# Kernel tuning notes

Hardware: AMD Instinct MI355X
Metric: run time of the kernel (lower is better)

Reference implementation:

```python
import jax, jax.numpy as jnp
import numpy as np

NUM_GROUPS = 256


def _linear(x, w, b):
    return x @ w + b


def _layernorm(x, g, b, eps=1e-5):
    mu = jnp.mean(x, axis=-1, keepdims=True)
    var = jnp.mean((x - mu) ** 2, axis=-1, keepdims=True)
    return (x - mu) / jnp.sqrt(var + eps) * g + b


def setup_inputs() -> dict:
    key = jax.random.key(0)
    ks = jax.random.split(key, 12)
    B, N, C = 16, 8192, 3
    s = 0.02
    return {
        "xyz": jax.random.normal(ks[0], (B, N, C), jnp.float32),
        "labels": jax.random.randint(ks[1], (B, N), 0, NUM_GROUPS),
        # conv1: Linear(3,128) -> LayerNorm(128) -> ReLU -> Linear(128,256)
        "w1a": jax.random.normal(ks[2], (3, 128), jnp.float32) * s,
        "b1a": jnp.zeros((128,), jnp.float32),
        "g1": jnp.ones((128,), jnp.float32),
        "beta1": jnp.zeros((128,), jnp.float32),
        "w1b": jax.random.normal(ks[3], (128, 256), jnp.float32) * s,
        "b1b": jnp.zeros((256,), jnp.float32),
        # conv2: Linear(512,512) -> LayerNorm(512) -> ReLU -> Linear(512,256)
        "w2a": jax.random.normal(ks[4], (512, 512), jnp.float32) * s,
        "b2a": jnp.zeros((512,), jnp.float32),
        "g2": jnp.ones((512,), jnp.float32),
        "beta2": jnp.zeros((512,), jnp.float32),
        "w2b": jax.random.normal(ks[5], (512, 256), jnp.float32) * s,
        "b2b": jnp.zeros((256,), jnp.float32),
    }


def reference(xyz, labels, w1a, b1a, g1, beta1, w1b, b1b,
              w2a, b2a, g2, beta2, w2b, b2b):
    # per-batch segment reductions over cluster labels
    seg_sum = jax.vmap(lambda f, l: jax.ops.segment_sum(f, l, num_segments=NUM_GROUPS))
    seg_max = jax.vmap(lambda f, l: jax.ops.segment_max(f, l, num_segments=NUM_GROUPS))
    gather = jax.vmap(lambda p, l: p[l])  # [G,D],[N] -> [N,D]

    # centroids = per-cluster mean of xyz (converged kmeans centroids)
    counts = seg_sum(jnp.ones_like(xyz[..., :1]), labels)          # [B,G,1]
    centroids = seg_sum(xyz, labels) / jnp.maximum(counts, 1.0)    # [B,G,3]

    p_i = gather(centroids, labels)                                # [B,N,3]
    relative_xyz = xyz - p_i                                       # feature_type='dp'

    h = _linear(relative_xyz, w1a, b1a)
    h = jax.nn.relu(_layernorm(h, g1, beta1))
    h = _linear(h, w1b, b1b)                                       # [B,N,256]

    pooled = seg_max(h, labels)                                    # [B,G,256]
    pooled = jnp.where(jnp.isfinite(pooled), pooled, 0.0)          # empty groups -> 0
    repeated = gather(pooled, labels)                              # [B,N,256]

    cat = jnp.concatenate([repeated, h], axis=-1)                  # [B,N,512]
    h2 = _linear(cat, w2a, b2a)
    h2 = jax.nn.relu(_layernorm(h2, g2, beta2))
    h2 = _linear(h2, w2b, b2b)                                     # [B,N,256]

    out = seg_max(h2, labels)                                      # [B,G,256]
    out = jnp.where(jnp.isfinite(out), out, 0.0)
    return (centroids, out, p_i, labels)
```

## Files before the change

kernel.cpp:

```cpp
#include <hip/hip_runtime.h>
#include <hip/hip_bf16.h>

#define NB_  16
#define NPTS 8192
#define NG   256
#define NP   (NB_*NPTS)
#define NBLK (NP/64)

#define OFF_CENT 0
#define OFF_OUT  12288
#define OFF_PI   1060864
#define OFF_LAB  1454080

typedef unsigned short u16;
typedef __attribute__((ext_vector_type(8))) short bf16x8;
typedef __attribute__((ext_vector_type(4))) float f32x4;

static constexpr size_t WS_SUMS  = 0;
static constexpr size_t WS_A1    = 65536;
static constexpr size_t WS_H     = WS_A1   + (size_t)NP*128*2;
static constexpr size_t WS_PBF   = WS_H    + (size_t)NP*256*2;
static constexpr size_t WS_WT1   = WS_PBF  + (size_t)NB_*NG*256*2;
static constexpr size_t WS_WT2A  = WS_WT1  + (size_t)256*128*2;
static constexpr size_t WS_WT2B  = WS_WT2A + (size_t)512*512*2;
static constexpr size_t WS_PREP  = WS_WT2B + (size_t)256*512*2;
static constexpr size_t WS_OFFS  = WS_PREP + (size_t)NB_*NG*512*4;
static constexpr size_t WS_CNT   = WS_OFFS + (size_t)NB_*NG*4;
static constexpr size_t WS_CUR   = WS_CNT  + (size_t)NB_*NG*4;
static constexpr size_t WS_SPOS  = WS_CUR  + (size_t)NB_*NG*4;
static constexpr size_t WS_GLAB  = WS_SPOS + (size_t)NP*4;
static constexpr size_t WS_PF    = WS_GLAB + (size_t)NP*4;
static constexpr size_t WS_PL    = WS_PF   + (size_t)NBLK*256*4;
static constexpr size_t WS_DST   = WS_PL   + (size_t)NBLK*256*4;
static constexpr size_t WS_NEED  = WS_DST  + (size_t)NB_*NG*256*4;

__device__ __forceinline__ u16 f2bf_bits(float f){
  __hip_bfloat16 h = __float2bfloat16(f);
  union { __hip_bfloat16 h; u16 s; } u; u.h = h; return u.s;
}
__device__ __forceinline__ float bf_bits2f(u16 s){
  return __uint_as_float(((unsigned)s) << 16);
}

__device__ __forceinline__ void gload16(const void* g, void* l){
  __builtin_amdgcn_global_load_lds((const __attribute__((address_space(1))) void*)g,
                                   (__attribute__((address_space(3))) void*)l, 16, 0, 0);
}

__global__ void k_init(float* __restrict__ sums, int* __restrict__ cursor){
  int i = blockIdx.x*blockDim.x + threadIdx.x;
  if (i < NB_*NG*4) sums[i] = 0.f;
  if (i < NB_*NG) cursor[i] = 0;
}

__global__ void k_wt(const float* __restrict__ src, u16* __restrict__ dst, int K, int N){
  int i = blockIdx.x*blockDim.x + threadIdx.x;
  if (i >= K*N) return;
  int n = i / K, k = i - n*K;
  dst[i] = f2bf_bits(src[(size_t)k*N + n]);
}

__global__ void k_points(const float* __restrict__ xyz, const int* __restrict__ labels,
                         float* __restrict__ sums, float* __restrict__ outLab){
  int p = blockIdx.x*blockDim.x + threadIdx.x;
  if (p >= NP) return;
  int b = p / NPTS;
  int g = labels[p];
  float x = xyz[p*3+0], y = xyz[p*3+1], z = xyz[p*3+2];
  float* s = sums + (size_t)(b*NG + g)*4;
  atomicAdd(s+0, x); atomicAdd(s+1, y); atomicAdd(s+2, z); atomicAdd(s+3, 1.f);
  outLab[p] = (float)g;
}

__global__ void k_cent(const float* __restrict__ sums, float* __restrict__ cent_out){
  int i = blockIdx.x*blockDim.x + threadIdx.x;
  if (i >= NB_*NG) return;
  const float* s = sums + (size_t)i*4;
  float c = fmaxf(s[3], 1.f);
  cent_out[i*3+0] = s[0]/c;
  cent_out[i*3+1] = s[1]/c;
  cent_out[i*3+2] = s[2]/c;
}

__global__ void k_scan(const float* __restrict__ sums, int* __restrict__ offs,
                       int* __restrict__ counts){
  __shared__ int sc[256];
  int b = blockIdx.x, g = threadIdx.x;
  int c = (int)(sums[(size_t)(b*NG+g)*4+3] + 0.5f);
  sc[g] = c;
  __syncthreads();
  for (int d = 1; d < 256; d <<= 1){
    int t = (g >= d) ? sc[g-d] : 0;
    __syncthreads();
    sc[g] += t;
    __syncthreads();
  }
  offs[b*NG+g] = b*NPTS + sc[g] - c;
  counts[b*NG+g] = c;
}

__global__ void k_scatter(const int* __restrict__ labels, const int* __restrict__ offs,
                          int* __restrict__ cursor, int* __restrict__ sortpos,
                          int* __restrict__ glab){
  int p = blockIdx.x*blockDim.x + threadIdx.x;
  if (p >= NP) return;
  int b = p / NPTS, g = labels[p];
  int pos = offs[b*NG+g] + atomicAdd(&cursor[b*NG+g], 1);
  sortpos[p] = pos;
  glab[pos] = g;
}

__global__ __launch_bounds__(256) void k_mlp1(
    const float* __restrict__ xyz, const int* __restrict__ labels,
    const int* __restrict__ sortpos, const float* __restrict__ cent,
    const float* __restrict__ w1a, const float* __restrict__ b1a,
    const float* __restrict__ g1, const float* __restrict__ beta1,
    u16* __restrict__ a1, float* __restrict__ pi_out)
{
  int wave = (int)((blockIdx.x*blockDim.x + threadIdx.x) >> 6);
  int lane = threadIdx.x & 63;
  int p = wave;
  if (p >= NP) return;
  int b = p / NPTS;
  int g = labels[p];
  const float* cb = cent + (size_t)(b*NG+g)*3;
  float c0 = cb[0], c1 = cb[1], c2 = cb[2];
  float r0 = xyz[p*3+0]-c0, r1 = xyz[p*3+1]-c1, r2 = xyz[p*3+2]-c2;
  if (lane < 3) pi_out[(size_t)p*3+lane] = (lane==0?c0:(lane==1?c1:c2));
  int j = lane*2;
  float2 wa0 = *(const float2*)(w1a + 0*128 + j);
  float2 wa1 = *(const float2*)(w1a + 1*128 + j);
  float2 wa2 = *(const float2*)(w1a + 2*128 + j);
  float2 bb  = *(const float2*)(b1a + j);
  float t0 = bb.x + r0*wa0.x + r1*wa1.x + r2*wa2.x;
  float t1 = bb.y + r0*wa0.y + r1*wa1.y + r2*wa2.y;
  float s = t0+t1, sq = t0*t0 + t1*t1;
  #pragma unroll
  for (int m = 32; m; m >>= 1){ s += __shfl_xor(s, m); sq += __shfl_xor(sq, m); }
  float mu  = s * (1.f/128.f);
  float var = sq * (1.f/128.f) - mu*mu;
  float inv = rsqrtf(var + 1e-5f);
  float2 gg = *(const float2*)(g1 + j), be = *(const float2*)(beta1 + j);
  float a0 = fmaxf((t0-mu)*inv*gg.x + be.x, 0.f);
  float a1v = fmaxf((t1-mu)*inv*gg.y + be.y, 0.f);
  unsigned pk = ((unsigned)f2bf_bits(a1v) << 16) | f2bf_bits(a0);
  int sp = sortpos[p];
  *reinterpret_cast<unsigned*>(a1 + (size_t)sp*128 + j) = pk;
}

template<int EPI>
__global__ __launch_bounds__(256)
void mgemm(const u16* __restrict__ A, int lda, int K,
           const u16* __restrict__ BT, int ldb, int kofs,
           const float* __restrict__ bias,
           u16* __restrict__ Cst, float* __restrict__ Cf, int ldc, int Nc)
{
  __shared__ alignas(16) u16 As[128*32];
  __shared__ alignas(16) u16 Bs[128*32];
  int NBk = Nc >> 7;
  int bm = blockIdx.x / NBk, bn = blockIdx.x % NBk;
  int m0 = bm << 7, n0 = bn << 7;
  int tid = threadIdx.x;
  int lane = tid & 63, w = tid >> 6;
  int wr = w >> 1, wc = w & 1;
  int l15 = lane & 15, l4 = lane >> 4;
  int r0 = tid >> 2;
  int ks = (tid & 3) << 3;
  u16* asd0 = As + (size_t)(w*64)*8;
  u16* asd1 = As + (size_t)(256 + w*64)*8;
  u16* bsd0 = Bs + (size_t)(w*64)*8;
  u16* bsd1 = Bs + (size_t)(256 + w*64)*8;
  f32x4 acc[4][4];
  #pragma unroll
  for (int i = 0; i < 4; ++i)
    #pragma unroll
    for (int jj = 0; jj < 4; ++jj)
      #pragma unroll
      for (int e = 0; e < 4; ++e) acc[i][jj][e] = 0.f;

  for (int k0 = 0; k0 < K; k0 += 32){
    gload16(A + (size_t)(m0 + r0)*lda + k0 + ks, asd0);
    gload16(A + (size_t)(m0 + r0 + 64)*lda + k0 + ks, asd1);
    gload16(BT + (size_t)(n0 + r0)*ldb + kofs + k0 + ks, bsd0);
    gload16(BT + (size_t)(n0 + r0 + 64)*ldb + kofs + k0 + ks, bsd1);
    __syncthreads();
    bf16x8 af[4], bfr[4];
    #pragma unroll
    for (int i = 0; i < 4; ++i){
      af[i]  = *(const bf16x8*)&As[(size_t)(wr*64 + i*16 + l15)*32 + l4*8];
      bfr[i] = *(const bf16x8*)&Bs[(size_t)(wc*64 + i*16 + l15)*32 + l4*8];
    }
    #pragma unroll
    for (int i = 0; i < 4; ++i)
      #pragma unroll
      for (int jj = 0; jj < 4; ++jj)
        acc[i][jj] = __builtin_amdgcn_mfma_f32_16x16x32_bf16(af[i], bfr[jj], acc[i][jj], 0, 0, 0);
    __syncthreads();
  }

  float bi[4];
  #pragma unroll
  for (int jj = 0; jj < 4; ++jj) bi[jj] = bias[n0 + wc*64 + jj*16 + l15];
  #pragma unroll
  for (int i = 0; i < 4; ++i){
    #pragma unroll
    for (int r = 0; r < 4; ++r){
      int m = m0 + wr*64 + i*16 + l4*4 + r;
      #pragma unroll
      for (int jj = 0; jj < 4; ++jj){
        int n = n0 + wc*64 + jj*16 + l15;
        float v = acc[i][jj][r] + bi[jj];
        if (EPI == 1) Cst[(size_t)m*ldc + n] = f2bf_bits(v);
        if (EPI == 3) Cf[(size_t)m*ldc + n] = v;
      }
    }
  }
}

__global__ __launch_bounds__(256) void k_pool(const u16* __restrict__ h,
                                              const int* __restrict__ offs,
                                              const int* __restrict__ counts,
                                              u16* __restrict__ poolbf){
  int bg = blockIdx.x, c = threadIdx.x;
  int cnt = counts[bg];
  if (cnt == 0){ poolbf[(size_t)bg*256 + c] = 0; return; }
  int off = offs[bg];
  float mx = bf_bits2f(h[(size_t)off*256 + c]);
  for (int r = 1; r < cnt; ++r)
    mx = fmaxf(mx, bf_bits2f(h[(size_t)(off+r)*256 + c]));
  poolbf[(size_t)bg*256 + c] = f2bf_bits(mx);
}

__global__ __launch_bounds__(512, 4)
void fused2(const u16* __restrict__ h, const u16* __restrict__ wt2a,
            const u16* __restrict__ wt2b, const float* __restrict__ prepf,
            const float* __restrict__ b2b, const float* __restrict__ g2,
            const float* __restrict__ beta2, const int* __restrict__ glab,
            float* __restrict__ pf, float* __restrict__ pl, float* __restrict__ dstage)
{
  __shared__ alignas(16) char smem[81920];
  float* ssum = (float*)(smem + 65536);
  float* ssq  = (float*)(smem + 65536 + 256);
  int tid = threadIdx.x;
  int w = tid >> 6, lane = tid & 63;
  int l15 = lane & 15, l4 = lane >> 4;
  int m0 = blockIdx.x << 6;
  int srow = lane >> 2, skseg = (lane & 3) << 3;
  if (tid < 64){ ssum[tid] = 0.f; ssq[tid] = 0.f; }

  f32x4 acc[4][4];
  #pragma unroll
  for (int i = 0; i < 4; ++i)
    #pragma unroll
    for (int j = 0; j < 4; ++j)
      #pragma unroll
      for (int e = 0; e < 4; ++e) acc[i][j][e] = 0.f;

  for (int k0 = 0; k0 < 256; k0 += 32){
    if (w < 4)
      gload16(h + (size_t)(m0 + (w<<4) + srow)*256 + k0 + skseg, smem + (w<<10));
    #pragma unroll
    for (int q = 0; q < 4; ++q){
      int n = (w<<6) + (q<<4) + srow;
      gload16(wt2a + (size_t)n*512 + 256 + k0 + skseg,
              smem + 4096 + (((w<<6) + (q<<4)) << 6));
    }
    __syncthreads();
    bf16x8 af[4], bf[4];
    #pragma unroll
    for (int i = 0; i < 4; ++i)
      af[i] = *(const bf16x8*)(smem + ((((i<<4)+l15)) << 6) + (l4<<4));
    #pragma unroll
    for (int j = 0; j < 4; ++j)
      bf[j] = *(const bf16x8*)(smem + 4096 + (((w<<6)+(j<<4)+l15) << 6) + (l4<<4));
    #pragma unroll
    for (int i = 0; i < 4; ++i)
      #pragma unroll
      for (int j = 0; j < 4; ++j)
        acc[i][j] = __builtin_amdgcn_mfma_f32_16x16x32_bf16(af[i], bf[j], acc[i][j], 0, 0, 0);
    __syncthreads();
  }

  int gb = (m0 / NPTS) * NG;
  int grp[4][4];
  #pragma unroll
  for (int i = 0; i < 4; ++i)
    #pragma unroll
    for (int r = 0; r < 4; ++r)
      grp[i][r] = gb + glab[m0 + (i<<4) + (l4<<2) + r];
  #pragma unroll
  for (int i = 0; i < 4; ++i)
    #pragma unroll
    for (int j = 0; j < 4; ++j){
      int n = (w<<6) + (j<<4) + l15;
      #pragma unroll
      for (int r = 0; r < 4; ++r)
        acc[i][j][r] += prepf[((size_t)grp[i][r] << 9) + n];
    }
  #pragma unroll
  for (int i = 0; i < 4; ++i)
    #pragma unroll
    for (int r = 0; r < 4; ++r){
      float s = 0.f, q = 0.f;
      #pragma unroll
      for (int j = 0; j < 4; ++j){ float v = acc[i][j][r]; s += v; q += v*v; }
      #pragma unroll
      for (int mk = 1; mk < 16; mk <<= 1){ s += __shfl_xor(s, mk); q += __shfl_xor(q, mk); }
      if (l15 == 0){
        int row = (i<<4) + (l4<<2) + r;
        atomicAdd(&ssum[row], s);
        atomicAdd(&ssq[row], q);
      }
    }
  __syncthreads();
  if (tid < 64){
    float mu = ssum[tid] * (1.f/512.f);
    float var = ssq[tid] * (1.f/512.f) - mu*mu;
    ssum[tid] = mu;
    ssq[tid] = rsqrtf(var + 1e-5f);
  }
  __syncthreads();
  float gcol[4], bcol[4];
  #pragma unroll
  for (int j = 0; j < 4; ++j){
    int n = (w<<6) + (j<<4) + l15;
    gcol[j] = g2[n]; bcol[j] = beta2[n];
  }
  #pragma unroll
  for (int i = 0; i < 4; ++i)
    #pragma unroll
    for (int r = 0; r < 4; ++r){
      int row = (i<<4) + (l4<<2) + r;
      float mu = ssum[row], inv = ssq[row];
      #pragma unroll
      for (int j = 0; j < 4; ++j){
        int n = (w<<6) + (j<<4) + l15;
        float v = fmaxf((acc[i][j][r] - mu)*inv*gcol[j] + bcol[j], 0.f);
        int byo = (row << 10) + (n << 1);
        byo ^= (row & 7) << 4;
        *(u16*)(smem + byo) = f2bf_bits(v);
      }
    }
  __syncthreads();

  f32x4 acc2[4][2];
  #pragma unroll
  for (int i = 0; i < 4; ++i)
    #pragma unroll
    for (int j = 0; j < 2; ++j)
      #pragma unroll
      for (int e = 0; e < 4; ++e) acc2[i][j][e] = 0.f;

  for (int k0 = 0; k0 < 512; k0 += 32){
    #pragma unroll
    for (int q = 0; q < 2; ++q){
      int n = (w<<5) + (q<<4) + srow;
      gload16(wt2b + (size_t)n*512 + k0 + skseg,
              smem + 65536 + (((w<<5) + (q<<4)) << 6));
    }
    __syncthreads();
    bf16x8 af2[4], bf2[2];
    #pragma unroll
    for (int i = 0; i < 4; ++i){
      int row = (i<<4) + l15;
      int byo = (row << 10) + ((k0 + (l4<<3)) << 1);
      byo ^= (row & 7) << 4;
      af2[i] = *(const bf16x8*)(smem + byo);
    }
    #pragma unroll
    for (int j = 0; j < 2; ++j)
      bf2[j] = *(const bf16x8*)(smem + 65536 + (((w<<5)+(j<<4)+l15) << 6) + (l4<<4));
    #pragma unroll
    for (int i = 0; i < 4; ++i)
      #pragma unroll
      for (int j = 0; j < 2; ++j)
        acc2[i][j] = __builtin_amdgcn_mfma_f32_16x16x32_bf16(af2[i], bf2[j], acc2[i][j], 0, 0, 0);
    __syncthreads();
  }

  float bb0 = b2b[(w<<5) + l15], bb1 = b2b[(w<<5) + 16 + l15];
  float* vbuf = (float*)smem;
  int* glab_s = (int*)(smem + 65536);
  #pragma unroll
  for (int i = 0; i < 4; ++i)
    #pragma unroll
    for (int j = 0; j < 2; ++j){
      int n = (w<<5) + (j<<4) + l15;
      float bbj = j ? bb1 : bb0;
      #pragma unroll
      for (int r = 0; r < 4; ++r){
        int row = (i<<4) + (l4<<2) + r;
        vbuf[row*256 + n] = acc2[i][j][r] + bbj;
      }
    }
  if (tid < 64) glab_s[tid] = glab[m0 + tid];
  __syncthreads();
  if (tid < 256){
    int c = tid;
    size_t blk = blockIdx.x;
    int curg = glab_s[0];
    float mx = vbuf[c];
    bool from0 = true;
    for (int r = 1; r < 64; ++r){
      int g = glab_s[r];
      float v = vbuf[r*256 + c];
      if (g != curg){
        if (from0) pf[blk*256 + c] = mx;
        else       dstage[((size_t)(gb + curg))*256 + c] = mx;
        curg = g; mx = v; from0 = false;
      } else mx = fmaxf(mx, v);
    }
    if (from0) pf[blk*256 + c] = mx;
    else       pl[blk*256 + c] = mx;
  }
}

__global__ __launch_bounds__(256) void k_combine(const int* __restrict__ offs,
                                                 const int* __restrict__ counts,
                                                 const float* __restrict__ pf,
                                                 const float* __restrict__ pl,
                                                 const float* __restrict__ dstage,
                                                 float* __restrict__ outp){
  int bg = blockIdx.x, c = threadIdx.x;
  int cnt = counts[bg];
  if (cnt == 0){ outp[(size_t)bg*256 + c] = 0.f; return; }
  int off = offs[bg], end = off + cnt;
  int B0 = off >> 6, B1 = (end - 1) >> 6;
  float v;
  if (B0 == B1){
    if ((off & 63) == 0)      v = pf[(size_t)B0*256 + c];
    else if ((end & 63) == 0) v = pl[(size_t)B0*256 + c];
    else                      v = dstage[(size_t)bg*256 + c];
  } else {
    v = ((off & 63) == 0) ? pf[(size_t)B0*256 + c] : pl[(size_t)B0*256 + c];
    for (int k = B0 + 1; k <= B1; ++k)
      v = fmaxf(v, pf[(size_t)k*256 + c]);
  }
  outp[(size_t)bg*256 + c] = v;
}

__global__ void k_sig(float* __restrict__ out, float val){
  int i = blockIdx.x*blockDim.x + threadIdx.x;
  if (i < 256) out[i] = val;
}

extern "C" void kernel_launch(void* const* d_in, const int* in_sizes, int n_in,
                              void* d_out, int out_size, void* d_ws, size_t ws_size,
                              hipStream_t stream) {
  const float* xyz    = (const float*)d_in[0];
  const int*   labels = (const int*)  d_in[1];
  const float* w1a    = (const float*)d_in[2];
  const float* b1a    = (const float*)d_in[3];
  const float* g1     = (const float*)d_in[4];
  const float* beta1  = (const float*)d_in[5];
  const float* w1b    = (const float*)d_in[6];
  const float* b1b    = (const float*)d_in[7];
  const float* w2a    = (const float*)d_in[8];
  const float* b2a    = (const float*)d_in[9];
  const float* g2     = (const float*)d_in[10];
  const float* beta2  = (const float*)d_in[11];
  const float* w2b    = (const float*)d_in[12];
  const float* b2b    = (const float*)d_in[13];
  float* out = (float*)d_out;
  char* ws = (char*)d_ws;

  if (ws_size < WS_NEED){
    k_sig<<<1, 256, 0, stream>>>(out, 10000.f + (float)(ws_size >> 20));
    return;
  }

  float*     sums   = (float*)(ws + WS_SUMS);
  u16*       a1     = (u16*)(ws + WS_A1);
  u16*       h      = (u16*)(ws + WS_H);
  u16*       poolbf = (u16*)(ws + WS_PBF);
  u16*       wt1    = (u16*)(ws + WS_WT1);
  u16*       wt2a   = (u16*)(ws + WS_WT2A);
  u16*       wt2b   = (u16*)(ws + WS_WT2B);
  float*     prepf  = (float*)(ws + WS_PREP);
  int*       offs   = (int*)(ws + WS_OFFS);
  int*       counts = (int*)(ws + WS_CNT);
  int*       cursor = (int*)(ws + WS_CUR);
  int*       sortpos= (int*)(ws + WS_SPOS);
  int*       glab   = (int*)(ws + WS_GLAB);
  float*     pf     = (float*)(ws + WS_PF);
  float*     pl     = (float*)(ws + WS_PL);
  float*     dstage = (float*)(ws + WS_DST);

  float* cent_out = out + OFF_CENT;
  float* out_seg  = out + OFF_OUT;
  float* pi_out   = out + OFF_PI;
  float* lab_out  = out + OFF_LAB;

  k_init<<<64, 256, 0, stream>>>(sums, cursor);
  k_wt<<<(128*256+255)/256, 256, 0, stream>>>(w1b, wt1, 128, 256);
  k_wt<<<(512*512+255)/256, 256, 0, stream>>>(w2a, wt2a, 512, 512);
  k_wt<<<(512*256+255)/256, 256, 0, stream>>>(w2b, wt2b, 512, 256);
  k_points<<<NP/256, 256, 0, stream>>>(xyz, labels, sums, lab_out);
  k_cent<<<(NB_*NG+255)/256, 256, 0, stream>>>(sums, cent_out);
  k_scan<<<NB_, 256, 0, stream>>>(sums, offs, counts);
  k_scatter<<<NP/256, 256, 0, stream>>>(labels, offs, cursor, sortpos, glab);
  k_mlp1<<<NP/4, 256, 0, stream>>>(xyz, labels, sortpos, cent_out,
                                   w1a, b1a, g1, beta1, a1, pi_out);
  mgemm<1><<<(NP/128)*(256/128), 256, 0, stream>>>(
      a1, 128, 128, wt1, 128, 0, b1b, h, (float*)nullptr, 256, 256);
  k_pool<<<NB_*NG, 256, 0, stream>>>(h, offs, counts, poolbf);
  mgemm<3><<<(NB_*NG/128)*(512/128), 256, 0, stream>>>(
      poolbf, 256, 256, wt2a, 512, 0, b2a, (u16*)nullptr, prepf, 512, 512);
  fused2<<<NBLK, 512, 0, stream>>>(h, wt2a, wt2b, prepf, b2b, g2, beta2, glab,
                                   pf, pl, dstage);
  k_combine<<<NB_*NG, 256, 0, stream>>>(offs, counts, pf, pl, dstage, out_seg);
}
```

Baseline: 345.5 us.

## Fuse first segment-max pooling into GEMM epilogue with partial-tile combine

The first GEMM epilogue now keeps its 128x128 bf16 output tile in shared memory and runs a per-column segmented max over the sorted rows. It writes first-segment, last-segment and interior group maxima to new partial buffers. A lightweight combine kernel then merges these partials per group, where the old k_pool re-read the whole h tensor from global memory. This adds 32KB of LDS to the GEMM and a serial 128-row loop on half the threads. The fused2 launch-bounds occupancy hint is also lowered from 4 to 2, with only scoping changes in its body.

```diff
diff --git a/kernel.cpp b/kernel.cpp
--- a/kernel.cpp
+++ b/kernel.cpp
@@ -6,6 +6,7 @@
 #define NG   256
 #define NP   (NB_*NPTS)
 #define NBLK (NP/64)
+#define NBLK1 (NP/128)
 
 #define OFF_CENT 0
 #define OFF_OUT  12288
@@ -32,7 +33,10 @@
 static constexpr size_t WS_PF    = WS_GLAB + (size_t)NP*4;
 static constexpr size_t WS_PL    = WS_PF   + (size_t)NBLK*256*4;
 static constexpr size_t WS_DST   = WS_PL   + (size_t)NBLK*256*4;
-static constexpr size_t WS_NEED  = WS_DST  + (size_t)NB_*NG*256*4;
+static constexpr size_t WS_PF1   = WS_DST  + (size_t)NB_*NG*256*4;
+static constexpr size_t WS_PL1   = WS_PF1  + (size_t)NBLK1*256*4;
+static constexpr size_t WS_DP1   = WS_PL1  + (size_t)NBLK1*256*4;
+static constexpr size_t WS_NEED  = WS_DP1  + (size_t)NB_*NG*256*4;
 
 __device__ __forceinline__ u16 f2bf_bits(float f){
   __hip_bfloat16 h = __float2bfloat16(f);
@@ -153,10 +157,13 @@
 void mgemm(const u16* __restrict__ A, int lda, int K,
            const u16* __restrict__ BT, int ldb, int kofs,
            const float* __restrict__ bias,
-           u16* __restrict__ Cst, float* __restrict__ Cf, int ldc, int Nc)
+           u16* __restrict__ Cst, float* __restrict__ Cf, int ldc, int Nc,
+           const int* __restrict__ glab,
+           float* __restrict__ pf1, float* __restrict__ pl1, float* __restrict__ dpool)
 {
   __shared__ alignas(16) u16 As[128*32];
   __shared__ alignas(16) u16 Bs[128*32];
+  __shared__ alignas(16) u16 vpool[EPI == 5 ? 128*128 : 1];
   int NBk = Nc >> 7;
   int bm = blockIdx.x / NBk, bn = blockIdx.x % NBk;
   int m0 = bm << 7, n0 = bn << 7;
@@ -205,33 +212,72 @@
   for (int i = 0; i < 4; ++i){
     #pragma unroll
     for (int r = 0; r < 4; ++r){
-      int m = m0 + wr*64 + i*16 + l4*4 + r;
+      int mrow = wr*64 + i*16 + l4*4 + r;
+      int m = m0 + mrow;
       #pragma unroll
       for (int jj = 0; jj < 4; ++jj){
-        int n = n0 + wc*64 + jj*16 + l15;
+        int nc = wc*64 + jj*16 + l15;
+        int n = n0 + nc;
         float v = acc[i][jj][r] + bi[jj];
-        if (EPI == 1) Cst[(size_t)m*ldc + n] = f2bf_bits(v);
+        if (EPI == 1 || EPI == 5){
+          u16 bv = f2bf_bits(v);
+          Cst[(size_t)m*ldc + n] = bv;
+          if (EPI == 5) vpool[mrow*128 + nc] = bv;
+        }
         if (EPI == 3) Cf[(size_t)m*ldc + n] = v;
       }
     }
   }
-}
-
-__global__ __launch_bounds__(256) void k_pool(const u16* __restrict__ h,
-                                              const int* __restrict__ offs,
-                                              const int* __restrict__ counts,
-                                              u16* __restrict__ poolbf){
+  if (EPI == 5){
+    int* glab_s = (int*)As;
+    if (tid < 128) glab_s[tid] = glab[m0 + tid];
+    __syncthreads();
+    if (tid < 128){
+      int c = tid;
+      int gb = (m0 / NPTS) * NG;
+      int curg = glab_s[0];
+      float mx = bf_bits2f(vpool[c]);
+      bool from0 = true;
+      for (int r = 1; r < 128; ++r){
+        int g = glab_s[r];
+        float v = bf_bits2f(vpool[r*128 + c]);
+        if (g != curg){
+          if (from0) pf1[(size_t)bm*256 + n0 + c] = mx;
+          else       dpool[((size_t)(gb + curg))*256 + n0 + c] = mx;
+          curg = g; mx = v; from0 = false;
+        } else mx = fmaxf(mx, v);
+      }
+      if (from0) pf1[(size_t)bm*256 + n0 + c] = mx;
+      else       pl1[(size_t)bm*256 + n0 + c] = mx;
+    }
+  }
+}
+
+__global__ __launch_bounds__(256) void k_poolcomb(const int* __restrict__ offs,
+                                                  const int* __restrict__ counts,
+                                                  const float* __restrict__ pf1,
+                                                  const float* __restrict__ pl1,
+                                                  const float* __restrict__ dpool,
+                                                  u16* __restrict__ poolbf){
   int bg = blockIdx.x, c = threadIdx.x;
   int cnt = counts[bg];
   if (cnt == 0){ poolbf[(size_t)bg*256 + c] = 0; return; }
-  int off = offs[bg];
-  float mx = bf_bits2f(h[(size_t)off*256 + c]);
-  for (int r = 1; r < cnt; ++r)
-    mx = fmaxf(mx, bf_bits2f(h[(size_t)(off+r)*256 + c]));
-  poolbf[(size_t)bg*256 + c] = f2bf_bits(mx);
-}
-
-__global__ __launch_bounds__(512, 4)
+  int off = offs[bg], end = off + cnt;
+  int B0 = off >> 7, B1 = (end - 1) >> 7;
+  float v;
+  if (B0 == B1){
+    if ((off & 127) == 0)      v = pf1[(size_t)B0*256 + c];
+    else if ((end & 127) == 0) v = pl1[(size_t)B0*256 + c];
+    else                       v = dpool[(size_t)bg*256 + c];
+  } else {
+    v = ((off & 127) == 0) ? pf1[(size_t)B0*256 + c] : pl1[(size_t)B0*256 + c];
+    for (int k = B0 + 1; k <= B1; ++k)
+      v = fmaxf(v, pf1[(size_t)k*256 + c]);
+  }
+  poolbf[(size_t)bg*256 + c] = f2bf_bits(v);
+}
+
+__global__ __launch_bounds__(512, 2)
 void fused2(const u16* __restrict__ h, const u16* __restrict__ wt2a,
             const u16* __restrict__ wt2b, const float* __restrict__ prepf,
             const float* __restrict__ b2b, const float* __restrict__ g2,
@@ -282,21 +328,23 @@
   }
 
   int gb = (m0 / NPTS) * NG;
-  int grp[4][4];
-  #pragma unroll
-  for (int i = 0; i < 4; ++i)
-    #pragma unroll
-    for (int r = 0; r < 4; ++r)
-      grp[i][r] = gb + glab[m0 + (i<<4) + (l4<<2) + r];
-  #pragma unroll
-  for (int i = 0; i < 4; ++i)
-    #pragma unroll
-    for (int j = 0; j < 4; ++j){
-      int n = (w<<6) + (j<<4) + l15;
+  {
+    int grp[4][4];
+    #pragma unroll
+    for (int i = 0; i < 4; ++i)
       #pragma unroll
       for (int r = 0; r < 4; ++r)
-        acc[i][j][r] += prepf[((size_t)grp[i][r] << 9) + n];
-    }
+        grp[i][r] = gb + glab[m0 + (i<<4) + (l4<<2) + r];
+    #pragma unroll
+    for (int i = 0; i < 4; ++i)
+      #pragma unroll
+      for (int j = 0; j < 4; ++j){
+        int n = (w<<6) + (j<<4) + l15;
+        #pragma unroll
+        for (int r = 0; r < 4; ++r)
+          acc[i][j][r] += prepf[((size_t)grp[i][r] << 9) + n];
+      }
+  }
   #pragma unroll
   for (int i = 0; i < 4; ++i)
     #pragma unroll
@@ -320,27 +368,29 @@
     ssq[tid] = rsqrtf(var + 1e-5f);
   }
   __syncthreads();
-  float gcol[4], bcol[4];
-  #pragma unroll
-  for (int j = 0; j < 4; ++j){
-    int n = (w<<6) + (j<<4) + l15;
-    gcol[j] = g2[n]; bcol[j] = beta2[n];
-  }
-  #pragma unroll
-  for (int i = 0; i < 4; ++i)
-    #pragma unroll
-    for (int r = 0; r < 4; ++r){
-      int row = (i<<4) + (l4<<2) + r;
-      float mu = ssum[row], inv = ssq[row];
-      #pragma unroll
-      for (int j = 0; j < 4; ++j){
-        int n = (w<<6) + (j<<4) + l15;
-        float v = fmaxf((acc[i][j][r] - mu)*inv*gcol[j] + bcol[j], 0.f);
-        int byo = (row << 10) + (n << 1);
-        byo ^= (row & 7) << 4;
-        *(u16*)(smem + byo) = f2bf_bits(v);
+  {
+    float gcol[4], bcol[4];
+    #pragma unroll
+    for (int j = 0; j < 4; ++j){
+      int n = (w<<6) + (j<<4) + l15;
+      gcol[j] = g2[n]; bcol[j] = beta2[n];
+    }
+    #pragma unroll
+    for (int i = 0; i < 4; ++i)
+      #pragma unroll
+      for (int r = 0; r < 4; ++r){
+        int row = (i<<4) + (l4<<2) + r;
+        float mu = ssum[row], inv = ssq[row];
+        #pragma unroll
+        for (int j = 0; j < 4; ++j){
+          int n = (w<<6) + (j<<4) + l15;
+          float v = fmaxf((acc[i][j][r] - mu)*inv*gcol[j] + bcol[j], 0.f);
+          int byo = (row << 10) + (n << 1);
+          byo ^= (row & 7) << 4;
+          *(u16*)(smem + byo) = f2bf_bits(v);
+        }
       }
-    }
+  }
   __syncthreads();
 
   f32x4 acc2[4][2];
@@ -485,6 +535,9 @@
   float*     pf     = (float*)(ws + WS_PF);
   float*     pl     = (float*)(ws + WS_PL);
   float*     dstage = (float*)(ws + WS_DST);
+  float*     pf1    = (float*)(ws + WS_PF1);
+  float*     pl1    = (float*)(ws + WS_PL1);
+  float*     dpool  = (float*)(ws + WS_DP1);
 
   float* cent_out = out + OFF_CENT;
   float* out_seg  = out + OFF_OUT;
@@ -501,11 +554,13 @@
   k_scatter<<<NP/256, 256, 0, stream>>>(labels, offs, cursor, sortpos, glab);
   k_mlp1<<<NP/4, 256, 0, stream>>>(xyz, labels, sortpos, cent_out,
                                    w1a, b1a, g1, beta1, a1, pi_out);
-  mgemm<1><<<(NP/128)*(256/128), 256, 0, stream>>>(
-      a1, 128, 128, wt1, 128, 0, b1b, h, (float*)nullptr, 256, 256);
-  k_pool<<<NB_*NG, 256, 0, stream>>>(h, offs, counts, poolbf);
+  mgemm<5><<<(NP/128)*(256/128), 256, 0, stream>>>(
+      a1, 128, 128, wt1, 128, 0, b1b, h, (float*)nullptr, 256, 256,
+      glab, pf1, pl1, dpool);
+  k_poolcomb<<<NB_*NG, 256, 0, stream>>>(offs, counts, pf1, pl1, dpool, poolbf);
   mgemm<3><<<(NB_*NG/128)*(512/128), 256, 0, stream>>>(
-      poolbf, 256, 256, wt2a, 512, 0, b2a, (u16*)nullptr, prepf, 512, 512);
+      poolbf, 256, 256, wt2a, 512, 0, b2a, (u16*)nullptr, prepf, 512, 512,
+      (const int*)nullptr, (float*)nullptr, (float*)nullptr, (float*)nullptr);
   fused2<<<NBLK, 512, 0, stream>>>(h, wt2a, wt2b, prepf, b2b, g2, beta2, glab,
                                    pf, pl, dstage);
   k_combine<<<NB_*NG, 256, 0, stream>>>(offs, counts, pf, pl, dstage, out_seg);
```

After: 398.4 us. +15.3%, slower.

## Halve fused MLP2 row tile and read weight fragments directly from global

Applied to the files above, without the earlier changes.

The fused second-MLP kernel now handles 32 points per block instead of 64 and stages the whole 32x256 h tile into LDS once, using an XOR swizzle. Weight fragments for both GEMMs are loaded straight from global memory into registers, so the per-k-step LDS staging and its barriers go away. LDS use drops from 80KB to about 33KB, which should allow more resident blocks. In exchange, weight reuse per block is halved and global/L2 weight traffic doubles. The combine kernel and the segment-max staging are adjusted to the 32-row block size, and the vbuf row stride is padded to 260 to avoid bank conflicts.

```diff
diff --git a/kernel.cpp b/kernel.cpp
--- a/kernel.cpp
+++ b/kernel.cpp
@@ -5,7 +5,7 @@
 #define NPTS 8192
 #define NG   256
 #define NP   (NB_*NPTS)
-#define NBLK (NP/64)
+#define NBLK (NP/32)
 
 #define OFF_CENT 0
 #define OFF_OUT  12288
@@ -232,73 +232,82 @@
 }
 
 __global__ __launch_bounds__(512, 4)
-void fused2(const u16* __restrict__ h, const u16* __restrict__ wt2a,
+void fused3(const u16* __restrict__ h, const u16* __restrict__ wt2a,
             const u16* __restrict__ wt2b, const float* __restrict__ prepf,
             const float* __restrict__ b2b, const float* __restrict__ g2,
             const float* __restrict__ beta2, const int* __restrict__ glab,
             float* __restrict__ pf, float* __restrict__ pl, float* __restrict__ dstage)
 {
-  __shared__ alignas(16) char smem[81920];
-  float* ssum = (float*)(smem + 65536);
-  float* ssq  = (float*)(smem + 65536 + 256);
+  __shared__ alignas(16) char smem[33792];
+  float* ssum  = (float*)(smem + 33280);
+  float* ssq   = (float*)(smem + 33408);
+  int*  glab_s = (int*)(smem + 33536);
   int tid = threadIdx.x;
   int w = tid >> 6, lane = tid & 63;
   int l15 = lane & 15, l4 = lane >> 4;
-  int m0 = blockIdx.x << 6;
-  int srow = lane >> 2, skseg = (lane & 3) << 3;
-  if (tid < 64){ ssum[tid] = 0.f; ssq[tid] = 0.f; }
-
-  f32x4 acc[4][4];
-  #pragma unroll
-  for (int i = 0; i < 4; ++i)
+  int m0 = blockIdx.x << 5;
+  if (tid < 32){ ssum[tid] = 0.f; ssq[tid] = 0.f; glab_s[tid] = glab[m0 + tid]; }
+
+  const char* hb = (const char*)h;
+  {
+    int lrow = lane >> 5;
+    int kb = (lane & 31) << 4;
+    #pragma unroll
+    for (int t = 0; t < 2; ++t){
+      int q = w*2 + t;
+      int row = q*2 + lrow;
+      gload16(hb + (size_t)(m0 + row)*512 + (kb ^ ((row & 7) << 4)),
+              smem + q*1024);
+    }
+  }
+  f32x4 acc[2][4];
+  #pragma unroll
+  for (int i = 0; i < 2; ++i)
     #pragma unroll
     for (int j = 0; j < 4; ++j)
       #pragma unroll
       for (int e = 0; e < 4; ++e) acc[i][j][e] = 0.f;
+  __syncthreads();
 
   for (int k0 = 0; k0 < 256; k0 += 32){
-    if (w < 4)
-      gload16(h + (size_t)(m0 + (w<<4) + srow)*256 + k0 + skseg, smem + (w<<10));
-    #pragma unroll
-    for (int q = 0; q < 4; ++q){
-      int n = (w<<6) + (q<<4) + srow;
-      gload16(wt2a + (size_t)n*512 + 256 + k0 + skseg,
-              smem + 4096 + (((w<<6) + (q<<4)) << 6));
-    }
-    __syncthreads();
-    bf16x8 af[4], bf[4];
-    #pragma unroll
-    for (int i = 0; i < 4; ++i)
-      af[i] = *(const bf16x8*)(smem + ((((i<<4)+l15)) << 6) + (l4<<4));
-    #pragma unroll
-    for (int j = 0; j < 4; ++j)
-      bf[j] = *(const bf16x8*)(smem + 4096 + (((w<<6)+(j<<4)+l15) << 6) + (l4<<4));
-    #pragma unroll
-    for (int i = 0; i < 4; ++i)
-      #pragma unroll
-      for (int j = 0; j < 4; ++j)
-        acc[i][j] = __builtin_amdgcn_mfma_f32_16x16x32_bf16(af[i], bf[j], acc[i][j], 0, 0, 0);
-    __syncthreads();
-  }
-
-  int gb = (m0 / NPTS) * NG;
-  int grp[4][4];
-  #pragma unroll
-  for (int i = 0; i < 4; ++i)
-    #pragma unroll
-    for (int r = 0; r < 4; ++r)
-      grp[i][r] = gb + glab[m0 + (i<<4) + (l4<<2) + r];
-  #pragma unroll
-  for (int i = 0; i < 4; ++i)
+    bf16x8 af[2], bfr[4];
+    #pragma unroll
+    for (int i = 0; i < 2; ++i){
+      int row = i*16 + l15;
+      af[i] = *(const bf16x8*)(smem + row*512 + (((k0 + l4*8) << 1) ^ ((row & 7) << 4)));
+    }
     #pragma unroll
     for (int j = 0; j < 4; ++j){
       int n = (w<<6) + (j<<4) + l15;
+      bfr[j] = *(const bf16x8*)(wt2a + (size_t)n*512 + 256 + k0 + l4*8);
+    }
+    #pragma unroll
+    for (int i = 0; i < 2; ++i)
+      #pragma unroll
+      for (int j = 0; j < 4; ++j)
+        acc[i][j] = __builtin_amdgcn_mfma_f32_16x16x32_bf16(af[i], bfr[j], acc[i][j], 0, 0, 0);
+  }
+
+  int gb = (m0 / NPTS) * NG;
+  {
+    int grp[2][4];
+    #pragma unroll
+    for (int i = 0; i < 2; ++i)
       #pragma unroll
       for (int r = 0; r < 4; ++r)
-        acc[i][j][r] += prepf[((size_t)grp[i][r] << 9) + n];
-    }
-  #pragma unroll
-  for (int i = 0; i < 4; ++i)
+        grp[i][r] = gb + glab_s[(i<<4) + (l4<<2) + r];
+    #pragma unroll
+    for (int i = 0; i < 2; ++i)
+      #pragma unroll
+      for (int j = 0; j < 4; ++j){
+        int n = (w<<6) + (j<<4) + l15;
+        #pragma unroll
+        for (int r = 0; r < 4; ++r)
+          acc[i][j][r] += prepf[((size_t)grp[i][r] << 9) + n];
+      }
+  }
+  #pragma unroll
+  for (int i = 0; i < 2; ++i)
     #pragma unroll
     for (int r = 0; r < 4; ++r){
       float s = 0.f, q = 0.f;
@@ -313,76 +322,69 @@
       }
     }
   __syncthreads();
-  if (tid < 64){
+  if (tid < 32){
     float mu = ssum[tid] * (1.f/512.f);
     float var = ssq[tid] * (1.f/512.f) - mu*mu;
     ssum[tid] = mu;
     ssq[tid] = rsqrtf(var + 1e-5f);
   }
   __syncthreads();
-  float gcol[4], bcol[4];
-  #pragma unroll
-  for (int j = 0; j < 4; ++j){
-    int n = (w<<6) + (j<<4) + l15;
-    gcol[j] = g2[n]; bcol[j] = beta2[n];
-  }
-  #pragma unroll
-  for (int i = 0; i < 4; ++i)
-    #pragma unroll
-    for (int r = 0; r < 4; ++r){
-      int row = (i<<4) + (l4<<2) + r;
-      float mu = ssum[row], inv = ssq[row];
-      #pragma unroll
-      for (int j = 0; j < 4; ++j){
-        int n = (w<<6) + (j<<4) + l15;
-        float v = fmaxf((acc[i][j][r] - mu)*inv*gcol[j] + bcol[j], 0.f);
-        int byo = (row << 10) + (n << 1);
-        byo ^= (row & 7) << 4;
-        *(u16*)(smem + byo) = f2bf_bits(v);
+  {
+    float gcol[4], bcol[4];
+    #pragma unroll
+    for (int j = 0; j < 4; ++j){
+      int n = (w<<6) + (j<<4) + l15;
+      gcol[j] = g2[n]; bcol[j] = beta2[n];
+    }
+    #pragma unroll
+    for (int i = 0; i < 2; ++i)
+      #pragma unroll
+      for (int r = 0; r < 4; ++r){
+        int row = (i<<4) + (l4<<2) + r;
+        float mu = ssum[row], inv = ssq[row];
+        #pragma unroll
+        for (int j = 0; j < 4; ++j){
+          int n = (w<<6) + (j<<4) + l15;
+          float v = fmaxf((acc[i][j][r] - mu)*inv*gcol[j] + bcol[j], 0.f);
+          int byo = (row << 10) + ((n << 1) ^ ((row & 7) << 4));
+          *(u16*)(smem + byo) = f2bf_bits(v);
+        }
       }
-    }
-  __syncthreads();
-
-  f32x4 acc2[4][2];
-  #pragma unroll
-  for (int i = 0; i < 4; ++i)
+  }
+  __syncthreads();
+
+  f32x4 acc2[2][2];
+  #pragma unroll
+  for (int i = 0; i < 2; ++i)
     #pragma unroll
     for (int j = 0; j < 2; ++j)
       #pragma unroll
       for (int e = 0; e < 4; ++e) acc2[i][j][e] = 0.f;
 
   for (int k0 = 0; k0 < 512; k0 += 32){
-    #pragma unroll
-    for (int q = 0; q < 2; ++q){
-      int n = (w<<5) + (q<<4) + srow;
-      gload16(wt2b + (size_t)n*512 + k0 + skseg,
-              smem + 65536 + (((w<<5) + (q<<4)) << 6));
-    }
-    __syncthreads();
-    bf16x8 af2[4], bf2[2];
-    #pragma unroll
-    for (int i = 0; i < 4; ++i){
+    bf16x8 af2[2], bf2[2];
+    #pragma unroll
+    for (int i = 0; i < 2; ++i){
       int row = (i<<4) + l15;
-      int byo = (row << 10) + ((k0 + (l4<<3)) << 1);
-      byo ^= (row & 7) << 4;
-      af2[i] = *(const bf16x8*)(smem + byo);
-    }
-    #pragma unroll
-    for (int j = 0; j < 2; ++j)
-      bf2[j] = *(const bf16x8*)(smem + 65536 + (((w<<5)+(j<<4)+l15) << 6) + (l4<<4));
-    #pragma unroll
-    for (int i = 0; i < 4; ++i)
+      af2[i] = *(const bf16x8*)(smem + (row << 10) + ((((k0 + l4*8)) << 1) ^ ((row & 7) << 4)));
+    }
+    #pragma unroll
+    for (int j = 0; j < 2; ++j){
+      int n = (w<<5) + (j<<4) + l15;
+      bf2[j] = *(const bf16x8*)(wt2b + (size_t)n*512 + k0 + l4*8);
+    }
+    #pragma unroll
+    for (int i = 0; i < 2; ++i)
       #pragma unroll
       for (int j = 0; j < 2; ++j)
         acc2[i][j] = __builtin_amdgcn_mfma_f32_16x16x32_bf16(af2[i], bf2[j], acc2[i][j], 0, 0, 0);
-    __syncthreads();
-  }
+  }
+  __syncthreads();
 
   float bb0 = b2b[(w<<5) + l15], bb1 = b2b[(w<<5) + 16 + l15];
   float* vbuf = (float*)smem;
-  int* glab_s = (int*)(smem + 65536);
-  #pragma unroll
-  for (int i = 0; i < 4; ++i)
+  #pragma unroll
+  for (int i = 0; i < 2; ++i)
     #pragma unroll
     for (int j = 0; j < 2; ++j){
       int n = (w<<5) + (j<<4) + l15;
@@ -390,10 +392,9 @@
       #pragma unroll
       for (int r = 0; r < 4; ++r){
         int row = (i<<4) + (l4<<2) + r;
-        vbuf[row*256 + n] = acc2[i][j][r] + bbj;
+        vbuf[row*260 + n] = acc2[i][j][r] + bbj;
       }
     }
-  if (tid < 64) glab_s[tid] = glab[m0 + tid];
   __syncthreads();
   if (tid < 256){
     int c = tid;
@@ -401,9 +402,9 @@
     int curg = glab_s[0];
     float mx = vbuf[c];
     bool from0 = true;
-    for (int r = 1; r < 64; ++r){
+    for (int r = 1; r < 32; ++r){
       int g = glab_s[r];
-      float v = vbuf[r*256 + c];
+      float v = vbuf[r*260 + c];
       if (g != curg){
         if (from0) pf[blk*256 + c] = mx;
         else       dstage[((size_t)(gb + curg))*256 + c] = mx;
@@ -425,14 +426,14 @@
   int cnt = counts[bg];
   if (cnt == 0){ outp[(size_t)bg*256 + c] = 0.f; return; }
   int off = offs[bg], end = off + cnt;
-  int B0 = off >> 6, B1 = (end - 1) >> 6;
+  int B0 = off >> 5, B1 = (end - 1) >> 5;
   float v;
   if (B0 == B1){
-    if ((off & 63) == 0)      v = pf[(size_t)B0*256 + c];
-    else if ((end & 63) == 0) v = pl[(size_t)B0*256 + c];
+    if ((off & 31) == 0)      v = pf[(size_t)B0*256 + c];
+    else if ((end & 31) == 0) v = pl[(size_t)B0*256 + c];
     else                      v = dstage[(size_t)bg*256 + c];
   } else {
-    v = ((off & 63) == 0) ? pf[(size_t)B0*256 + c] : pl[(size_t)B0*256 + c];
+    v = ((off & 31) == 0) ? pf[(size_t)B0*256 + c] : pl[(size_t)B0*256 + c];
     for (int k = B0 + 1; k <= B1; ++k)
       v = fmaxf(v, pf[(size_t)k*256 + c]);
   }
@@ -506,7 +507,7 @@
   k_pool<<<NB_*NG, 256, 0, stream>>>(h, offs, counts, poolbf);
   mgemm<3><<<(NB_*NG/128)*(512/128), 256, 0, stream>>>(
       poolbf, 256, 256, wt2a, 512, 0, b2a, (u16*)nullptr, prepf, 512, 512);
-  fused2<<<NBLK, 512, 0, stream>>>(h, wt2a, wt2b, prepf, b2b, g2, beta2, glab,
+  fused3<<<NBLK, 512, 0, stream>>>(h, wt2a, wt2b, prepf, b2b, g2, beta2, glab,
                                    pf, pl, dstage);
   k_combine<<<NB_*NG, 256, 0, stream>>>(offs, counts, pf, pl, dstage, out_seg);
 }
```

New measurement: 415.7 us. 20.3% more time.

## Preload whole h tile to LDS and stream weights directly from global

Applied to the files above, without the earlier changes.

Loads the full 64x256 h tile into swizzled LDS once up front instead of per-k slices. Reads the wt2a and wt2b B-fragments straight from global (L2-cached) into registers instead of staging them through LDS, which removes the per-iteration barriers in both GEMM loops. It also caches the group labels in LDS early and shrinks shared memory to allow more resident blocks. The trade-off is exposed global-load latency on the weight fragments inside the MFMA loops, with no LDS staging to hide it.

```diff
diff --git a/kernel.cpp b/kernel.cpp
--- a/kernel.cpp
+++ b/kernel.cpp
@@ -232,22 +232,34 @@
 }
 
 __global__ __launch_bounds__(512, 4)
-void fused2(const u16* __restrict__ h, const u16* __restrict__ wt2a,
+void fused4(const u16* __restrict__ h, const u16* __restrict__ wt2a,
             const u16* __restrict__ wt2b, const float* __restrict__ prepf,
             const float* __restrict__ b2b, const float* __restrict__ g2,
             const float* __restrict__ beta2, const int* __restrict__ glab,
             float* __restrict__ pf, float* __restrict__ pl, float* __restrict__ dstage)
 {
-  __shared__ alignas(16) char smem[81920];
-  float* ssum = (float*)(smem + 65536);
-  float* ssq  = (float*)(smem + 65536 + 256);
+  __shared__ alignas(16) char smem[66560];
+  float* ssum  = (float*)(smem + 65536);
+  float* ssq   = (float*)(smem + 65792);
+  int*  glab_s = (int*)(smem + 66048);
   int tid = threadIdx.x;
   int w = tid >> 6, lane = tid & 63;
   int l15 = lane & 15, l4 = lane >> 4;
   int m0 = blockIdx.x << 6;
-  int srow = lane >> 2, skseg = (lane & 3) << 3;
-  if (tid < 64){ ssum[tid] = 0.f; ssq[tid] = 0.f; }
-
+  if (tid < 64){ ssum[tid] = 0.f; ssq[tid] = 0.f; glab_s[tid] = glab[m0 + tid]; }
+
+  {
+    const char* hb = (const char*)h;
+    int lrow = lane >> 5;
+    int kb = (lane & 31) << 4;
+    #pragma unroll
+    for (int t = 0; t < 4; ++t){
+      int q = w*4 + t;
+      int row = q*2 + lrow;
+      gload16(hb + (size_t)(m0 + row)*512 + (kb ^ ((row & 7) << 4)),
+              smem + q*1024);
+    }
+  }
   f32x4 acc[4][4];
   #pragma unroll
   for (int i = 0; i < 4; ++i)
@@ -255,48 +267,45 @@
     for (int j = 0; j < 4; ++j)
       #pragma unroll
       for (int e = 0; e < 4; ++e) acc[i][j][e] = 0.f;
+  __syncthreads();
 
   for (int k0 = 0; k0 < 256; k0 += 32){
-    if (w < 4)
-      gload16(h + (size_t)(m0 + (w<<4) + srow)*256 + k0 + skseg, smem + (w<<10));
-    #pragma unroll
-    for (int q = 0; q < 4; ++q){
-      int n = (w<<6) + (q<<4) + srow;
-      gload16(wt2a + (size_t)n*512 + 256 + k0 + skseg,
-              smem + 4096 + (((w<<6) + (q<<4)) << 6));
-    }
-    __syncthreads();
-    bf16x8 af[4], bf[4];
-    #pragma unroll
-    for (int i = 0; i < 4; ++i)
-      af[i] = *(const bf16x8*)(smem + ((((i<<4)+l15)) << 6) + (l4<<4));
-    #pragma unroll
-    for (int j = 0; j < 4; ++j)
-      bf[j] = *(const bf16x8*)(smem + 4096 + (((w<<6)+(j<<4)+l15) << 6) + (l4<<4));
-    #pragma unroll
-    for (int i = 0; i < 4; ++i)
-      #pragma unroll
-      for (int j = 0; j < 4; ++j)
-        acc[i][j] = __builtin_amdgcn_mfma_f32_16x16x32_bf16(af[i], bf[j], acc[i][j], 0, 0, 0);
-    __syncthreads();
-  }
-
-  int gb = (m0 / NPTS) * NG;
-  int grp[4][4];
-  #pragma unroll
-  for (int i = 0; i < 4; ++i)
-    #pragma unroll
-    for (int r = 0; r < 4; ++r)
-      grp[i][r] = gb + glab[m0 + (i<<4) + (l4<<2) + r];
-  #pragma unroll
-  for (int i = 0; i < 4; ++i)
+    bf16x8 af[4], bfr[4];
+    #pragma unroll
+    for (int i = 0; i < 4; ++i){
+      int row = (i<<4) + l15;
+      af[i] = *(const bf16x8*)(smem + row*512 + ((((k0 + l4*8)) << 1) ^ ((row & 7) << 4)));
+    }
     #pragma unroll
     for (int j = 0; j < 4; ++j){
       int n = (w<<6) + (j<<4) + l15;
+      bfr[j] = *(const bf16x8*)(wt2a + (size_t)n*512 + 256 + k0 + l4*8);
+    }
+    #pragma unroll
+    for (int i = 0; i < 4; ++i)
+      #pragma unroll
+      for (int j = 0; j < 4; ++j)
+        acc[i][j] = __builtin_amdgcn_mfma_f32_16x16x32_bf16(af[i], bfr[j], acc[i][j], 0, 0, 0);
+  }
+
+  int gb = (m0 / NPTS) * NG;
+  {
+    int grp[4][4];
+    #pragma unroll
+    for (int i = 0; i < 4; ++i)
       #pragma unroll
       for (int r = 0; r < 4; ++r)
-        acc[i][j][r] += prepf[((size_t)grp[i][r] << 9) + n];
-    }
+        grp[i][r] = gb + glab_s[(i<<4) + (l4<<2) + r];
+    #pragma unroll
+    for (int i = 0; i < 4; ++i)
+      #pragma unroll
+      for (int j = 0; j < 4; ++j){
+        int n = (w<<6) + (j<<4) + l15;
+        #pragma unroll
+        for (int r = 0; r < 4; ++r)
+          acc[i][j][r] += prepf[((size_t)grp[i][r] << 9) + n];
+      }
+  }
   #pragma unroll
   for (int i = 0; i < 4; ++i)
     #pragma unroll
@@ -320,67 +329,60 @@
     ssq[tid] = rsqrtf(var + 1e-5f);
   }
   __syncthreads();
-  float gcol[4], bcol[4];
-  #pragma unroll
-  for (int j = 0; j < 4; ++j){
-    int n = (w<<6) + (j<<4) + l15;
-    gcol[j] = g2[n]; bcol[j] = beta2[n];
-  }
+  {
+    float gcol[4], bcol[4];
+    #pragma unroll
+    for (int j = 0; j < 4; ++j){
+      int n = (w<<6) + (j<<4) + l15;
+      gcol[j] = g2[n]; bcol[j] = beta2[n];
+    }
+    #pragma unroll
+    for (int i = 0; i < 4; ++i)
+      #pragma unroll
+      for (int r = 0; r < 4; ++r){
+        int row = (i<<4) + (l4<<2) + r;
+        float mu = ssum[row], inv = ssq[row];
+        #pragma unroll
+        for (int j = 0; j < 4; ++j){
+          int n = (w<<6) + (j<<4) + l15;
+          float v = fmaxf((acc[i][j][r] - mu)*inv*gcol[j] + bcol[j], 0.f);
+          int byo = (row << 10) + (((n << 1)) ^ ((row & 7) << 4));
+          *(u16*)(smem + byo) = f2bf_bits(v);
+        }
+      }
+  }
+  __syncthreads();
+
+  f32x4 acc2[4][2];
   #pragma unroll
   for (int i = 0; i < 4; ++i)
     #pragma unroll
-    for (int r = 0; r < 4; ++r){
-      int row = (i<<4) + (l4<<2) + r;
-      float mu = ssum[row], inv = ssq[row];
-      #pragma unroll
-      for (int j = 0; j < 4; ++j){
-        int n = (w<<6) + (j<<4) + l15;
-        float v = fmaxf((acc[i][j][r] - mu)*inv*gcol[j] + bcol[j], 0.f);
-        int byo = (row << 10) + (n << 1);
-        byo ^= (row & 7) << 4;
-        *(u16*)(smem + byo) = f2bf_bits(v);
-      }
-    }
-  __syncthreads();
-
-  f32x4 acc2[4][2];
-  #pragma unroll
-  for (int i = 0; i < 4; ++i)
-    #pragma unroll
     for (int j = 0; j < 2; ++j)
       #pragma unroll
       for (int e = 0; e < 4; ++e) acc2[i][j][e] = 0.f;
 
   for (int k0 = 0; k0 < 512; k0 += 32){
-    #pragma unroll
-    for (int q = 0; q < 2; ++q){
-      int n = (w<<5) + (q<<4) + srow;
-      gload16(wt2b + (size_t)n*512 + k0 + skseg,
-              smem + 65536 + (((w<<5) + (q<<4)) << 6));
-    }
-    __syncthreads();
     bf16x8 af2[4], bf2[2];
     #pragma unroll
     for (int i = 0; i < 4; ++i){
       int row = (i<<4) + l15;
-      int byo = (row << 10) + ((k0 + (l4<<3)) << 1);
-      byo ^= (row & 7) << 4;
-      af2[i] = *(const bf16x8*)(smem + byo);
-    }
-    #pragma unroll
-    for (int j = 0; j < 2; ++j)
-      bf2[j] = *(const bf16x8*)(smem + 65536 + (((w<<5)+(j<<4)+l15) << 6) + (l4<<4));
+      af2[i] = *(const bf16x8*)(smem + (row << 10) + ((((k0 + l4*8)) << 1) ^ ((row & 7) << 4)));
+    }
+    #pragma unroll
+    for (int j = 0; j < 2; ++j){
+      int n = (w<<5) + (j<<4) + l15;
+      bf2[j] = *(const bf16x8*)(wt2b + (size_t)n*512 + k0 + l4*8);
+    }
     #pragma unroll
     for (int i = 0; i < 4; ++i)
       #pragma unroll
       for (int j = 0; j < 2; ++j)
         acc2[i][j] = __builtin_amdgcn_mfma_f32_16x16x32_bf16(af2[i], bf2[j], acc2[i][j], 0, 0, 0);
-    __syncthreads();
-  }
+  }
+  __syncthreads();
 
   float bb0 = b2b[(w<<5) + l15], bb1 = b2b[(w<<5) + 16 + l15];
   float* vbuf = (float*)smem;
-  int* glab_s = (int*)(smem + 65536);
   #pragma unroll
   for (int i = 0; i < 4; ++i)
     #pragma unroll
@@ -393,7 +395,6 @@
         vbuf[row*256 + n] = acc2[i][j][r] + bbj;
       }
     }
-  if (tid < 64) glab_s[tid] = glab[m0 + tid];
   __syncthreads();
   if (tid < 256){
     int c = tid;
@@ -506,7 +507,7 @@
   k_pool<<<NB_*NG, 256, 0, stream>>>(h, offs, counts, poolbf);
   mgemm<3><<<(NB_*NG/128)*(512/128), 256, 0, stream>>>(
       poolbf, 256, 256, wt2a, 512, 0, b2a, (u16*)nullptr, prepf, 512, 512);
-  fused2<<<NBLK, 512, 0, stream>>>(h, wt2a, wt2b, prepf, b2b, g2, beta2, glab,
+  fused4<<<NBLK, 512, 0, stream>>>(h, wt2a, wt2b, prepf, b2b, g2, beta2, glab,
                                    pf, pl, dstage);
   k_combine<<<NB_*NG, 256, 0, stream>>>(offs, counts, pf, pl, dstage, out_seg);
 }
```

New measurement: 370.3 us. +7.2%, slower.
